# Performance work log

Measured on AMD Instinct MI355X. Metric: run time of the kernel, lower is better.

## Reference

```python
import jax, jax.numpy as jnp
import numpy as np

N_NODES = 100000
N_EDGES = 1600000
N_FEAT = 128
HIDDEN = 128
N_CLASSES = 64


def setup_inputs() -> dict:
    key = jax.random.key(0)
    ks = jax.random.split(key, 6)
    x = jax.random.normal(ks[0], (N_NODES, N_FEAT), dtype=jnp.float32)
    edge_index = jax.random.randint(ks[1], (2, N_EDGES), 0, N_NODES, dtype=jnp.int64)
    # Glorot-ish scaled weights
    W1_l = jax.random.normal(ks[2], (N_FEAT, HIDDEN), dtype=jnp.float32) / np.sqrt(N_FEAT)
    W1_r = jax.random.normal(ks[3], (N_FEAT, HIDDEN), dtype=jnp.float32) / np.sqrt(N_FEAT)
    W2_l = jax.random.normal(ks[4], (HIDDEN, N_CLASSES), dtype=jnp.float32) / np.sqrt(HIDDEN)
    W2_r = jax.random.normal(ks[5], (HIDDEN, N_CLASSES), dtype=jnp.float32) / np.sqrt(HIDDEN)
    b1 = jnp.zeros((HIDDEN,), dtype=jnp.float32)
    b2 = jnp.zeros((N_CLASSES,), dtype=jnp.float32)
    return {"x": x, "edge_index": edge_index, "W1_l": W1_l, "b1": b1,
            "W1_r": W1_r, "W2_l": W2_l, "b2": b2, "W2_r": W2_r}


def _sage_conv(h, src, dst, n_nodes, inv_deg, W_l, W_r, b):
    # mean aggregation of source-node features into destination nodes
    agg = jax.ops.segment_sum(h[src], dst, num_segments=n_nodes)  # [N, d]
    agg = agg * inv_deg[:, None]
    return agg @ W_l + h @ W_r + b


def reference(x, edge_index, W1_l, b1, W1_r, W2_l, b2, W2_r):
    src, dst = edge_index[0], edge_index[1]
    n = x.shape[0]
    deg = jax.ops.segment_sum(jnp.ones_like(dst, dtype=x.dtype), dst, num_segments=n)
    inv_deg = 1.0 / jnp.maximum(deg, 1.0)
    h = jax.nn.relu(_sage_conv(x, src, dst, n, inv_deg, W1_l, W1_r, b1))
    # dropout is identity in eval mode
    out = _sage_conv(h, src, dst, n, inv_deg, W2_l, W2_r, b2)
    return out
```

## Files before the change

### kernel.cpp

```cpp
#include <hip/hip_runtime.h>

#define N_NODES   100000
#define N_EDGES   1600000
#define BSHIFT    9
#define NB        196
#define BSTRIDE   9216

typedef __attribute__((ext_vector_type(8))) short short8;
typedef __attribute__((ext_vector_type(4))) float f32x4;
typedef __attribute__((ext_vector_type(2))) float f32x2;

__device__ __forceinline__ unsigned short f2bf(float f) {
    unsigned u = __float_as_uint(f);
    u += 0x7FFF + ((u >> 16) & 1);
    return (unsigned short)(u >> 16);
}

__device__ __forceinline__ int load_src(const int* e, int is64, int i) {
    return is64 ? e[2 * i] : e[i];
}
__device__ __forceinline__ int load_dst(const int* e, int is64, int i) {
    return is64 ? e[2 * (N_EDGES + i)] : e[N_EDGES + i];
}

__device__ __forceinline__ int block_detect_is64(const int* e, int* s_nz) {
    if (threadIdx.x == 0) *s_nz = 0;
    __syncthreads();
    int v = 0;
    for (int i = threadIdx.x; i < 1024; i += 256) v |= e[2 * i + 1];
    if (v) atomicOr(s_nz, 1);
    __syncthreads();
    return (*s_nz == 0) ? 1 : 0;
}

__global__ __launch_bounds__(256) void phaseA_kernel(
        const int* __restrict__ e, const float* __restrict__ x,
        const float* __restrict__ W1_l, const float* __restrict__ W1_r,
        const float* __restrict__ W2_l, const float* __restrict__ W2_r,
        int* __restrict__ bktcur, int* __restrict__ pairs,
        short* __restrict__ xb, unsigned int* __restrict__ xq,
        short* __restrict__ W1t, short* __restrict__ W2lt, short* __restrict__ W2rt) {
    __shared__ int2 s_pairs[4096];
    __shared__ int s_cnt[256], s_off[256], s_base[256], s_cur[256];
    __shared__ int s_nz;
    const int blk = blockIdx.x;
    if (blk < 391) {
        const int tid = threadIdx.x;
        s_cnt[tid] = 0;
        int is64 = block_detect_is64(e, &s_nz);
        __syncthreads();
        int i0 = blk * 4096;
        int n = min(4096, N_EDGES - i0);
        int ls[16], ld[16];
        #pragma unroll
        for (int t = 0; t < 16; t++) {
            int k = t * 256 + tid;
            if (k < n) {
                ls[t] = load_src(e, is64, i0 + k);
                ld[t] = load_dst(e, is64, i0 + k);
                atomicAdd(&s_cnt[ld[t] >> BSHIFT], 1);
            }
        }
        __syncthreads();
        int lv = s_cnt[tid];
        s_off[tid] = lv;
        __syncthreads();
        for (int off = 1; off < 256; off <<= 1) {
            int t = (tid >= off) ? s_off[tid - off] : 0;
            __syncthreads();
            s_off[tid] += t;
            __syncthreads();
        }
        int excl = s_off[tid] - lv;
        int gb = 0;
        if (tid < NB && lv > 0) gb = atomicAdd(&bktcur[tid], lv);
        s_off[tid] = excl;
        s_base[tid] = tid * BSTRIDE + gb;
        s_cur[tid] = excl;
        __syncthreads();
        #pragma unroll
        for (int t = 0; t < 16; t++) {
            int k = t * 256 + tid;
            if (k < n) {
                int pos = atomicAdd(&s_cur[ld[t] >> BSHIFT], 1);
                s_pairs[pos] = (int2){ls[t], ld[t]};
            }
        }
        __syncthreads();
        for (int j = tid; j < n; j += 256) {
            int2 pr = s_pairs[j];
            int b = pr.y >> BSHIFT;
            pairs[s_base[b] + (j - s_off[b])] = pr.x | ((pr.y & 511) << 17);
        }
    } else if (blk < 12891) {
        int t = (blk - 391) * 256 + threadIdx.x;
        int i = t * 4;
        float4 v = *(const float4*)&x[i];
        short4 o;
        o.x = (short)f2bf(v.x); o.y = (short)f2bf(v.y);
        o.z = (short)f2bf(v.z); o.w = (short)f2bf(v.w);
        *(short4*)&xb[i] = o;
        int w = __builtin_amdgcn_cvt_pk_fp8_f32(v.x, v.y, 0, false);
        w = __builtin_amdgcn_cvt_pk_fp8_f32(v.z, v.w, w, true);
        xq[t] = (unsigned int)w;
    } else {
        int i = (blk - 12891) * 256 + threadIdx.x;
        if (i < 32768) {
            int n = i >> 8, k = i & 255;
            float v = (k < 128) ? W1_l[k * 128 + n] : W1_r[(k - 128) * 128 + n];
            W1t[i] = (short)f2bf(v);
        } else if (i < 40960) {
            int j = i - 32768, n = j >> 7, k = j & 127;
            W2lt[j] = (short)f2bf(W2_l[k * 64 + n]);
        } else {
            int j = i - 40960, n = j >> 7, k = j & 127;
            W2rt[j] = (short)f2bf(W2_r[k * 64 + n]);
        }
    }
}

__global__ __launch_bounds__(512) void fused_fill_kernel(
        const int* __restrict__ bktcur, const int* __restrict__ pairs,
        int* __restrict__ deg_i, int* __restrict__ cursor,
        float* __restrict__ inv_deg, int* __restrict__ col) {
    __shared__ int ldeg[512];
    __shared__ int ssum[512];
    const int tid = threadIdx.x;
    const int b = blockIdx.x;
    const int nbase = b << BSHIFT;
    ldeg[tid] = 0;
    __syncthreads();
    const int cnt = bktcur[b];
    const int p0 = b * BSTRIDE;
    for (int j = tid; j < cnt; j += 512)
        atomicAdd(&ldeg[pairs[p0 + j] >> 17], 1);
    __syncthreads();
    int d = ldeg[tid];
    ssum[tid] = d;
    __syncthreads();
    for (int off = 1; off < 512; off <<= 1) {
        int t = (tid >= off) ? ssum[tid - off] : 0;
        __syncthreads();
        ssum[tid] += t;
        __syncthreads();
    }
    int s = p0 + ssum[tid] - d;
    int node = nbase + tid;
    if (node < N_NODES) {
        deg_i[node] = d;
        cursor[node] = s;
        inv_deg[node] = 1.0f / fmaxf((float)d, 1.0f);
    }
    ldeg[tid] = s;
    __syncthreads();
    for (int j = tid; j < cnt; j += 512) {
        int pk = pairs[p0 + j];
        int pos = atomicAdd(&ldeg[pk >> 17], 1);
        col[pos] = pk & 0x1FFFF;
    }
}

__device__ __forceinline__ void acc_fp8x8(float* acc, uint2 w) {
    f32x2 f;
    f = __builtin_amdgcn_cvt_pk_f32_fp8((int)w.x, false); acc[0] += f[0]; acc[1] += f[1];
    f = __builtin_amdgcn_cvt_pk_f32_fp8((int)w.x, true);  acc[2] += f[0]; acc[3] += f[1];
    f = __builtin_amdgcn_cvt_pk_f32_fp8((int)w.y, false); acc[4] += f[0]; acc[5] += f[1];
    f = __builtin_amdgcn_cvt_pk_f32_fp8((int)w.y, true);  acc[6] += f[0]; acc[7] += f[1];
}

__global__ __launch_bounds__(256) void agg128_kernel(
        const int* __restrict__ cursor, const int* __restrict__ deg_i,
        const int* __restrict__ col, const unsigned int* __restrict__ xq,
        const float* __restrict__ inv_deg, short* __restrict__ agg) {
    int node = blockIdx.x * 16 + (threadIdx.x >> 4);
    int lane = threadIdx.x & 15;
    int cnt = deg_i[node];
    int start = cursor[node];
    float acc[8] = {0.f};
    int k = 0;
    for (; k + 4 <= cnt; k += 4) {
        int s0 = col[start + k + 0];
        int s1 = col[start + k + 1];
        int s2 = col[start + k + 2];
        int s3 = col[start + k + 3];
        uint2 w0 = *(const uint2*)(xq + (size_t)s0 * 32 + lane * 2);
        uint2 w1 = *(const uint2*)(xq + (size_t)s1 * 32 + lane * 2);
        uint2 w2 = *(const uint2*)(xq + (size_t)s2 * 32 + lane * 2);
        uint2 w3 = *(const uint2*)(xq + (size_t)s3 * 32 + lane * 2);
        acc_fp8x8(acc, w0); acc_fp8x8(acc, w1);
        acc_fp8x8(acc, w2); acc_fp8x8(acc, w3);
    }
    for (; k < cnt; k++) {
        int s0 = col[start + k];
        uint2 w = *(const uint2*)(xq + (size_t)s0 * 32 + lane * 2);
        acc_fp8x8(acc, w);
    }
    float sc = inv_deg[node];
    short8 o;
    #pragma unroll
    for (int j = 0; j < 8; j++) o[j] = (short)f2bf(acc[j] * sc);
    *(short8*)(agg + (size_t)node * 128 + lane * 8) = o;
}

__global__ __launch_bounds__(256) void agg64_kernel(
        const int* __restrict__ cursor, const int* __restrict__ deg_i,
        const int* __restrict__ col, const unsigned int* __restrict__ pq,
        const float* __restrict__ inv_deg, float* __restrict__ out) {
    int node = blockIdx.x * 32 + (threadIdx.x >> 3);
    int lane = threadIdx.x & 7;
    int cnt = deg_i[node];
    int start = cursor[node];
    float acc[8] = {0.f};
    int k = 0;
    for (; k + 4 <= cnt; k += 4) {
        int s0 = col[start + k + 0];
        int s1 = col[start + k + 1];
        int s2 = col[start + k + 2];
        int s3 = col[start + k + 3];
        uint2 w0 = *(const uint2*)(pq + (size_t)s0 * 16 + lane * 2);
        uint2 w1 = *(const uint2*)(pq + (size_t)s1 * 16 + lane * 2);
        uint2 w2 = *(const uint2*)(pq + (size_t)s2 * 16 + lane * 2);
        uint2 w3 = *(const uint2*)(pq + (size_t)s3 * 16 + lane * 2);
        acc_fp8x8(acc, w0); acc_fp8x8(acc, w1);
        acc_fp8x8(acc, w2); acc_fp8x8(acc, w3);
    }
    for (; k < cnt; k++) {
        int s0 = col[start + k];
        uint2 w = *(const uint2*)(pq + (size_t)s0 * 16 + lane * 2);
        acc_fp8x8(acc, w);
    }
    float sc = inv_deg[node];
    float* dst = out + (size_t)node * 64 + lane * 8;
    float4 o0 = *(float4*)dst;
    float4 o1 = *(float4*)(dst + 4);
    o0.x += acc[0] * sc; o0.y += acc[1] * sc; o0.z += acc[2] * sc; o0.w += acc[3] * sc;
    o1.x += acc[4] * sc; o1.y += acc[5] * sc; o1.z += acc[6] * sc; o1.w += acc[7] * sc;
    *(float4*)dst = o0;
    *(float4*)(dst + 4) = o1;
}

__global__ __launch_bounds__(256, 2) void gemm1_mfma(
        const short* __restrict__ agg1, const short* __restrict__ xb,
        const short* __restrict__ W1t, const float* __restrict__ b1,
        short* __restrict__ h) {
    const int wave = threadIdx.x >> 6, lane = threadIdx.x & 63;
    const int m = lane & 15, q = lane >> 4;
    const int wid = blockIdx.x * 4 + wave;
    const int half = wid & 1;
    short8 breg[4][8];
    #pragma unroll
    for (int t = 0; t < 4; t++)
        #pragma unroll
        for (int c = 0; c < 8; c++)
            breg[t][c] = *(const short8*)(W1t + (size_t)(half * 64 + t * 16 + m) * 256 + c * 32 + q * 8);
    float bias[4];
    #pragma unroll
    for (int t = 0; t < 4; t++) bias[t] = b1[half * 64 + t * 16 + m];

    int tile = wid >> 1;
    if (tile >= 6250) return;
    short8 a[8];
    {
        const short* arow = agg1 + (size_t)(tile * 16 + m) * 128;
        const short* xrow = xb + (size_t)(tile * 16 + m) * 128;
        #pragma unroll
        for (int c = 0; c < 4; c++) {
            a[c]     = *(const short8*)(arow + c * 32 + q * 8);
            a[c + 4] = *(const short8*)(xrow + c * 32 + q * 8);
        }
    }
    while (true) {
        int nt = tile + 1024;
        short8 an[8];
        if (nt < 6250) {
            const short* arow = agg1 + (size_t)(nt * 16 + m) * 128;
            const short* xrow = xb + (size_t)(nt * 16 + m) * 128;
            #pragma unroll
            for (int c = 0; c < 4; c++) {
                an[c]     = *(const short8*)(arow + c * 32 + q * 8);
                an[c + 4] = *(const short8*)(xrow + c * 32 + q * 8);
            }
        }
        f32x4 acc[4];
        #pragma unroll
        for (int t = 0; t < 4; t++) acc[t] = (f32x4){0.f, 0.f, 0.f, 0.f};
        #pragma unroll
        for (int c = 0; c < 8; c++)
            #pragma unroll
            for (int t = 0; t < 4; t++)
                acc[t] = __builtin_amdgcn_mfma_f32_16x16x32_bf16(a[c], breg[t][c], acc[t], 0, 0, 0);
        #pragma unroll
        for (int t = 0; t < 4; t++) {
            int colc = half * 64 + t * 16 + m;
            #pragma unroll
            for (int r = 0; r < 4; r++) {
                int rr = tile * 16 + q * 4 + r;
                h[(size_t)rr * 128 + colc] = (short)f2bf(fmaxf(acc[t][r] + bias[t], 0.f));
            }
        }
        if (nt >= 6250) break;
        #pragma unroll
        for (int c = 0; c < 8; c++) a[c] = an[c];
        tile = nt;
    }
}

__global__ __launch_bounds__(256, 2) void proj2_mfma(
        const short* __restrict__ h, const short* __restrict__ W2lt,
        const short* __restrict__ W2rt, const float* __restrict__ b2,
        unsigned char* __restrict__ p8, float* __restrict__ out) {
    const int wave = threadIdx.x >> 6, lane = threadIdx.x & 63;
    const int m = lane & 15, q = lane >> 4;
    const int wid = blockIdx.x * 4 + wave;
    short8 bl[4][4], br[4][4];
    #pragma unroll
    for (int t = 0; t < 4; t++)
        #pragma unroll
        for (int c = 0; c < 4; c++) {
            bl[t][c] = *(const short8*)(W2lt + (size_t)(t * 16 + m) * 128 + c * 32 + q * 8);
            br[t][c] = *(const short8*)(W2rt + (size_t)(t * 16 + m) * 128 + c * 32 + q * 8);
        }
    float bias[4];
    #pragma unroll
    for (int t = 0; t < 4; t++) bias[t] = b2[t * 16 + m];

    int tile = wid;
    if (tile >= 6250) return;
    short8 a[4];
    {
        const short* hrow = h + (size_t)(tile * 16 + m) * 128;
        #pragma unroll
        for (int c = 0; c < 4; c++) a[c] = *(const short8*)(hrow + c * 32 + q * 8);
    }
    while (true) {
        int nt = tile + 2048;
        short8 an[4];
        if (nt < 6250) {
            const short* hrow = h + (size_t)(nt * 16 + m) * 128;
            #pragma unroll
            for (int c = 0; c < 4; c++) an[c] = *(const short8*)(hrow + c * 32 + q * 8);
        }
        f32x4 accp[4], acco[4];
        #pragma unroll
        for (int t = 0; t < 4; t++) {
            accp[t] = (f32x4){0.f, 0.f, 0.f, 0.f};
            acco[t] = (f32x4){0.f, 0.f, 0.f, 0.f};
        }
        #pragma unroll
        for (int c = 0; c < 4; c++)
            #pragma unroll
            for (int t = 0; t < 4; t++) {
                accp[t] = __builtin_amdgcn_mfma_f32_16x16x32_bf16(a[c], bl[t][c], accp[t], 0, 0, 0);
                acco[t] = __builtin_amdgcn_mfma_f32_16x16x32_bf16(a[c], br[t][c], acco[t], 0, 0, 0);
            }
        #pragma unroll
        for (int t = 0; t < 4; t++) {
            int colc = t * 16 + m;
            #pragma unroll
            for (int r = 0; r < 4; r++) {
                int rr = tile * 16 + q * 4 + r;
                float pv = accp[t][r];
                int w = __builtin_amdgcn_cvt_pk_fp8_f32(pv, pv, 0, false);
                p8[(size_t)rr * 64 + colc] = (unsigned char)(w & 0xFF);
                out[(size_t)rr * 64 + colc] = acco[t][r] + bias[t];
            }
        }
        if (nt >= 6250) break;
        #pragma unroll
        for (int c = 0; c < 4; c++) a[c] = an[c];
        tile = nt;
    }
}

extern "C" void kernel_launch(void* const* d_in, const int* in_sizes, int n_in,
                              void* d_out, int out_size, void* d_ws, size_t ws_size,
                              hipStream_t stream) {
    const float* x    = (const float*)d_in[0];
    const int*   edge = (const int*)d_in[1];
    const float* W1_l = (const float*)d_in[2];
    const float* b1   = (const float*)d_in[3];
    const float* W1_r = (const float*)d_in[4];
    const float* W2_l = (const float*)d_in[5];
    const float* b2   = (const float*)d_in[6];
    const float* W2_r = (const float*)d_in[7];
    float* out = (float*)d_out;

    int* iw = (int*)d_ws;
    int* deg_i  = iw;
    int* cursor = iw + 100000;
    int* bktcur = iw + 200000;
    float* inv_deg = (float*)(iw + 200256);
    int* col    = iw + 300352;
    short* xb   = (short*)(iw + 2106688);
    short* hb   = xb + 12800000;
    short* ag1  = hb + 12800000;
    short* W1t  = ag1 + 12800000;
    short* W2lt = W1t + 32768;
    short* W2rt = W2lt + 8192;
    unsigned int* xq = (unsigned int*)hb;
    int* pairs = (int*)ag1;
    unsigned char* p8 = (unsigned char*)ag1;
    unsigned int*  pq = (unsigned int*)ag1;

    hipMemsetAsync(bktcur, 0, 256 * sizeof(int), stream);

    phaseA_kernel<<<13083, 256, 0, stream>>>(edge, x, W1_l, W1_r, W2_l, W2_r,
                                             bktcur, pairs, xb, xq, W1t, W2lt, W2rt);
    fused_fill_kernel<<<NB, 512, 0, stream>>>(bktcur, pairs, deg_i, cursor, inv_deg, col);

    agg128_kernel<<<6250, 256, 0, stream>>>(cursor, deg_i, col, xq, inv_deg, ag1);
    gemm1_mfma<<<512, 256, 0, stream>>>(ag1, xb, W1t, b1, hb);

    proj2_mfma<<<512, 256, 0, stream>>>(hb, W2lt, W2rt, b2, p8, out);
    agg64_kernel<<<3125, 256, 0, stream>>>(cursor, deg_i, col, pq, inv_deg, out);
}
```

Before: 246.3 us.

## Fuse layer-1 GEMM and layer-2 projection through swizzled LDS tile

Merges the layer-1 dense GEMM (agg@W1_l + x@W1_r, relu) and the layer-2 projections into one kernel. Each block computes a 32-row h tile, stores it as bf16 in double-buffered, XOR-swizzled shared memory, then immediately multiplies it by W2_l/W2_r. The goal is to drop the global write and re-read of the 100000x128 bf16 hidden matrix and one kernel launch. In exchange each wave holds fewer weight columns, needs a block barrier per tile, and the p8 buffer is moved to the freed h region.

```diff
diff --git a/kernel.cpp b/kernel.cpp
--- a/kernel.cpp
+++ b/kernel.cpp
@@ -239,136 +239,138 @@
     *(float4*)(dst + 4) = o1;
 }
 
-__global__ __launch_bounds__(256, 2) void gemm1_mfma(
+__global__ __launch_bounds__(256, 2) void gemm12_mfma(
         const short* __restrict__ agg1, const short* __restrict__ xb,
         const short* __restrict__ W1t, const float* __restrict__ b1,
-        short* __restrict__ h) {
+        const short* __restrict__ W2lt, const short* __restrict__ W2rt,
+        const float* __restrict__ b2,
+        unsigned char* __restrict__ p8, float* __restrict__ out) {
+    __shared__ __align__(16) char hs[2][8192];
     const int wave = threadIdx.x >> 6, lane = threadIdx.x & 63;
     const int m = lane & 15, q = lane >> 4;
-    const int wid = blockIdx.x * 4 + wave;
-    const int half = wid & 1;
-    short8 breg[4][8];
+
+    short8 breg[2][8];
     #pragma unroll
-    for (int t = 0; t < 4; t++)
+    for (int t = 0; t < 2; t++)
         #pragma unroll
         for (int c = 0; c < 8; c++)
-            breg[t][c] = *(const short8*)(W1t + (size_t)(half * 64 + t * 16 + m) * 256 + c * 32 + q * 8);
-    float bias[4];
+            breg[t][c] = *(const short8*)(W1t + (size_t)(wave * 32 + t * 16 + m) * 256 + c * 32 + q * 8);
+    float bias1[2];
+    bias1[0] = b1[wave * 32 + m];
+    bias1[1] = b1[wave * 32 + 16 + m];
+
+    const int pw = wave & 1;
+    const short* Wp = (wave < 2) ? W2lt : W2rt;
+    short8 w2[2][4];
     #pragma unroll
-    for (int t = 0; t < 4; t++) bias[t] = b1[half * 64 + t * 16 + m];
-
-    int tile = wid >> 1;
-    if (tile >= 6250) return;
-    short8 a[8];
-    {
-        const short* arow = agg1 + (size_t)(tile * 16 + m) * 128;
-        const short* xrow = xb + (size_t)(tile * 16 + m) * 128;
+    for (int t = 0; t < 2; t++)
+        #pragma unroll
+        for (int c = 0; c < 4; c++)
+            w2[t][c] = *(const short8*)(Wp + (size_t)(pw * 32 + t * 16 + m) * 128 + c * 32 + q * 8);
+    float bias2[2];
+    bias2[0] = b2[pw * 32 + m];
+    bias2[1] = b2[pw * 32 + 16 + m];
+
+    int P = blockIdx.x;
+    short8 a[2][8];
+    #pragma unroll
+    for (int tt = 0; tt < 2; tt++) {
+        const short* arow = agg1 + (size_t)((2 * P + tt) * 16 + m) * 128;
+        const short* xrow = xb   + (size_t)((2 * P + tt) * 16 + m) * 128;
         #pragma unroll
         for (int c = 0; c < 4; c++) {
-            a[c]     = *(const short8*)(arow + c * 32 + q * 8);
-            a[c + 4] = *(const short8*)(xrow + c * 32 + q * 8);
-        }
-    }
+            a[tt][c]     = *(const short8*)(arow + c * 32 + q * 8);
+            a[tt][c + 4] = *(const short8*)(xrow + c * 32 + q * 8);
+        }
+    }
+    const int wb = wave * 64 + m * 2;
+    const int rsw = (m & 7) << 4;
+    int buf = 0;
     while (true) {
-        int nt = tile + 1024;
-        short8 an[8];
-        if (nt < 6250) {
-            const short* arow = agg1 + (size_t)(nt * 16 + m) * 128;
-            const short* xrow = xb + (size_t)(nt * 16 + m) * 128;
-            #pragma unroll
-            for (int c = 0; c < 4; c++) {
-                an[c]     = *(const short8*)(arow + c * 32 + q * 8);
-                an[c + 4] = *(const short8*)(xrow + c * 32 + q * 8);
+        f32x4 acc[2][2];
+        #pragma unroll
+        for (int tt = 0; tt < 2; tt++)
+            #pragma unroll
+            for (int t = 0; t < 2; t++) acc[tt][t] = (f32x4){0.f, 0.f, 0.f, 0.f};
+        #pragma unroll
+        for (int c = 0; c < 8; c++)
+            #pragma unroll
+            for (int tt = 0; tt < 2; tt++)
+                #pragma unroll
+                for (int t = 0; t < 2; t++)
+                    acc[tt][t] = __builtin_amdgcn_mfma_f32_16x16x32_bf16(a[tt][c], breg[t][c], acc[tt][t], 0, 0, 0);
+        int Pn = P + 512;
+        if (Pn < 3125) {
+            #pragma unroll
+            for (int tt = 0; tt < 2; tt++) {
+                const short* arow = agg1 + (size_t)((2 * Pn + tt) * 16 + m) * 128;
+                const short* xrow = xb   + (size_t)((2 * Pn + tt) * 16 + m) * 128;
+                #pragma unroll
+                for (int c = 0; c < 4; c++) {
+                    a[tt][c]     = *(const short8*)(arow + c * 32 + q * 8);
+                    a[tt][c + 4] = *(const short8*)(xrow + c * 32 + q * 8);
+                }
             }
         }
-        f32x4 acc[4];
-        #pragma unroll
-        for (int t = 0; t < 4; t++) acc[t] = (f32x4){0.f, 0.f, 0.f, 0.f};
-        #pragma unroll
-        for (int c = 0; c < 8; c++)
-            #pragma unroll
-            for (int t = 0; t < 4; t++)
-                acc[t] = __builtin_amdgcn_mfma_f32_16x16x32_bf16(a[c], breg[t][c], acc[t], 0, 0, 0);
-        #pragma unroll
-        for (int t = 0; t < 4; t++) {
-            int colc = half * 64 + t * 16 + m;
-            #pragma unroll
-            for (int r = 0; r < 4; r++) {
-                int rr = tile * 16 + q * 4 + r;
-                h[(size_t)rr * 128 + colc] = (short)f2bf(fmaxf(acc[t][r] + bias[t], 0.f));
-            }
-        }
-        if (nt >= 6250) break;
-        #pragma unroll
-        for (int c = 0; c < 8; c++) a[c] = an[c];
-        tile = nt;
-    }
-}
-
-__global__ __launch_bounds__(256, 2) void proj2_mfma(
-        const short* __restrict__ h, const short* __restrict__ W2lt,
-        const short* __restrict__ W2rt, const float* __restrict__ b2,
-        unsigned char* __restrict__ p8, float* __restrict__ out) {
-    const int wave = threadIdx.x >> 6, lane = threadIdx.x & 63;
-    const int m = lane & 15, q = lane >> 4;
-    const int wid = blockIdx.x * 4 + wave;
-    short8 bl[4][4], br[4][4];
-    #pragma unroll
-    for (int t = 0; t < 4; t++)
-        #pragma unroll
-        for (int c = 0; c < 4; c++) {
-            bl[t][c] = *(const short8*)(W2lt + (size_t)(t * 16 + m) * 128 + c * 32 + q * 8);
-            br[t][c] = *(const short8*)(W2rt + (size_t)(t * 16 + m) * 128 + c * 32 + q * 8);
-        }
-    float bias[4];
-    #pragma unroll
-    for (int t = 0; t < 4; t++) bias[t] = b2[t * 16 + m];
-
-    int tile = wid;
-    if (tile >= 6250) return;
-    short8 a[4];
-    {
-        const short* hrow = h + (size_t)(tile * 16 + m) * 128;
-        #pragma unroll
-        for (int c = 0; c < 4; c++) a[c] = *(const short8*)(hrow + c * 32 + q * 8);
-    }
-    while (true) {
-        int nt = tile + 2048;
-        short8 an[4];
-        if (nt < 6250) {
-            const short* hrow = h + (size_t)(nt * 16 + m) * 128;
-            #pragma unroll
-            for (int c = 0; c < 4; c++) an[c] = *(const short8*)(hrow + c * 32 + q * 8);
-        }
-        f32x4 accp[4], acco[4];
-        #pragma unroll
-        for (int t = 0; t < 4; t++) {
-            accp[t] = (f32x4){0.f, 0.f, 0.f, 0.f};
-            acco[t] = (f32x4){0.f, 0.f, 0.f, 0.f};
-        }
-        #pragma unroll
-        for (int c = 0; c < 4; c++)
-            #pragma unroll
-            for (int t = 0; t < 4; t++) {
-                accp[t] = __builtin_amdgcn_mfma_f32_16x16x32_bf16(a[c], bl[t][c], accp[t], 0, 0, 0);
-                acco[t] = __builtin_amdgcn_mfma_f32_16x16x32_bf16(a[c], br[t][c], acco[t], 0, 0, 0);
-            }
-        #pragma unroll
-        for (int t = 0; t < 4; t++) {
-            int colc = t * 16 + m;
-            #pragma unroll
-            for (int r = 0; r < 4; r++) {
-                int rr = tile * 16 + q * 4 + r;
-                float pv = accp[t][r];
-                int w = __builtin_amdgcn_cvt_pk_fp8_f32(pv, pv, 0, false);
-                p8[(size_t)rr * 64 + colc] = (unsigned char)(w & 0xFF);
-                out[(size_t)rr * 64 + colc] = acco[t][r] + bias[t];
-            }
-        }
-        if (nt >= 6250) break;
-        #pragma unroll
-        for (int c = 0; c < 4; c++) a[c] = an[c];
-        tile = nt;
+        char* hb0 = hs[buf];
+        #pragma unroll
+        for (int tt = 0; tt < 2; tt++)
+            #pragma unroll
+            for (int t = 0; t < 2; t++)
+                #pragma unroll
+                for (int r = 0; r < 4; r++) {
+                    int row = tt * 16 + q * 4 + r;
+                    int byteoff = row * 256 + ((wb + t * 32) ^ ((row & 7) << 4));
+                    float v = fmaxf(acc[tt][t][r] + bias1[t], 0.f);
+                    *(short*)(hb0 + byteoff) = (short)f2bf(v);
+                }
+        __syncthreads();
+        f32x4 acc2[2][2];
+        #pragma unroll
+        for (int tt = 0; tt < 2; tt++) {
+            short8 a2[4];
+            int rowbyte = (tt * 16 + m) * 256;
+            #pragma unroll
+            for (int c = 0; c < 4; c++)
+                a2[c] = *(const short8*)(hb0 + rowbyte + ((q * 16 + c * 64) ^ rsw));
+            #pragma unroll
+            for (int t = 0; t < 2; t++) acc2[tt][t] = (f32x4){0.f, 0.f, 0.f, 0.f};
+            #pragma unroll
+            for (int c = 0; c < 4; c++)
+                #pragma unroll
+                for (int t = 0; t < 2; t++)
+                    acc2[tt][t] = __builtin_amdgcn_mfma_f32_16x16x32_bf16(a2[c], w2[t][c], acc2[tt][t], 0, 0, 0);
+        }
+        if (wave < 2) {
+            #pragma unroll
+            for (int tt = 0; tt < 2; tt++)
+                #pragma unroll
+                for (int t = 0; t < 2; t++) {
+                    int colc = pw * 32 + t * 16 + m;
+                    #pragma unroll
+                    for (int r = 0; r < 4; r++) {
+                        int rr = (2 * P + tt) * 16 + q * 4 + r;
+                        float pv = acc2[tt][t][r];
+                        int w8 = __builtin_amdgcn_cvt_pk_fp8_f32(pv, pv, 0, false);
+                        p8[(size_t)rr * 64 + colc] = (unsigned char)(w8 & 0xFF);
+                    }
+                }
+        } else {
+            #pragma unroll
+            for (int tt = 0; tt < 2; tt++)
+                #pragma unroll
+                for (int t = 0; t < 2; t++) {
+                    int colc = pw * 32 + t * 16 + m;
+                    #pragma unroll
+                    for (int r = 0; r < 4; r++) {
+                        int rr = (2 * P + tt) * 16 + q * 4 + r;
+                        out[(size_t)rr * 64 + colc] = acc2[tt][t][r] + bias2[t];
+                    }
+                }
+        }
+        if (Pn >= 3125) break;
+        P = Pn;
+        buf ^= 1;
     }
 }
 
@@ -399,8 +401,8 @@
     short* W2rt = W2lt + 8192;
     unsigned int* xq = (unsigned int*)hb;
     int* pairs = (int*)ag1;
-    unsigned char* p8 = (unsigned char*)ag1;
-    unsigned int*  pq = (unsigned int*)ag1;
+    unsigned char* p8 = (unsigned char*)hb;
+    unsigned int*  pq = (unsigned int*)hb;
 
     hipMemsetAsync(bktcur, 0, 256 * sizeof(int), stream);
 
@@ -409,8 +411,6 @@
     fused_fill_kernel<<<NB, 512, 0, stream>>>(bktcur, pairs, deg_i, cursor, inv_deg, col);
 
     agg128_kernel<<<6250, 256, 0, stream>>>(cursor, deg_i, col, xq, inv_deg, ag1);
-    gemm1_mfma<<<512, 256, 0, stream>>>(ag1, xb, W1t, b1, hb);
-
-    proj2_mfma<<<512, 256, 0, stream>>>(hb, W2lt, W2rt, b2, p8, out);
+    gemm12_mfma<<<512, 256, 0, stream>>>(ag1, xb, W1t, b1, W2lt, W2rt, b2, p8, out);
     agg64_kernel<<<3125, 256, 0, stream>>>(cursor, deg_i, col, pq, inv_deg, out);
 }
```

Measured after the change: 239.6 us. -2.7%, faster.
